# Optimization experiments

Measured on AMD Instinct MI355X. Metric: run time of the kernel, lower is better.

Reference implementation:

```python
import jax, jax.numpy as jnp
import numpy as np
from jax import lax

BN_EPS = 1e-5


def setup_inputs() -> dict:
    key = jax.random.key(0)
    k1, k2 = jax.random.split(key)
    B, C, H, Wd = 32, 256, 56, 56
    x = jax.random.normal(k1, (B, C, H, Wd), dtype=jnp.float32)
    W = jax.random.normal(k2, (C, C, 3, 3), dtype=jnp.float32) * 0.05  # conv weight OIHW
    gamma = jnp.ones((C,), dtype=jnp.float32)
    beta = jnp.zeros((C,), dtype=jnp.float32)
    return {"x": x, "W": W, "gamma": gamma, "beta": beta}


def reference(x, W, gamma, beta):
    # sign activation on input, sign-binarized weights
    s = jnp.sign(x)
    bw = jnp.sign(W)
    # 3x3 conv, stride 1, padding 1 (same spatial size)
    y = lax.conv_general_dilated(
        s, bw,
        window_strides=(1, 1),
        padding=((1, 1), (1, 1)),
        dimension_numbers=("NCHW", "OIHW", "NCHW"),
    )
    # BatchNorm2d in training mode: batch statistics over (N, H, W), biased variance
    mean = jnp.mean(y, axis=(0, 2, 3))
    var = jnp.var(y, axis=(0, 2, 3))
    inv = gamma / jnp.sqrt(var + BN_EPS)
    yn = (y - mean[None, :, None, None]) * inv[None, :, None, None] + beta[None, :, None, None]
    return yn + x
```

## Files before the change

kernel.cpp:

```cpp
#include <hip/hip_runtime.h>
#include <stdint.h>

#define CH 256
#define HWD 56
#define POS 3136
#define BATCH 32
#define PP 3364
#define BN 128
#define NCH 26

typedef unsigned long long u64;
typedef __attribute__((ext_vector_type(4))) int  i32x4;
typedef __attribute__((ext_vector_type(16))) int i32x16;
typedef __attribute__((ext_vector_type(8))) short short8;

#define GLL16(gsrc, ldst) \
    __builtin_amdgcn_global_load_lds((const __attribute__((address_space(1))) void*)(gsrc), \
                                     (__attribute__((address_space(3))) void*)(ldst), 16, 0, 0)

__global__ __launch_bounds__(256) void pack_kernel(
        const float* __restrict__ x, const float* __restrict__ W,
        char* __restrict__ Xp, char* __restrict__ Wb2){
    int blk = blockIdx.x, t = threadIdx.x;
    if (blk < 144){
        int idx = blk*256 + t;
        int cc = idx & 15;
        int ot = idx >> 4;
        int o = ot / 9, tap = ot % 9;
        char v16[16];
        #pragma unroll
        for (int j=0;j<16;j++){
            float v = W[(size_t)(o*CH + cc*16 + j)*9 + tap];
            v16[j] = (v >= 0.f) ? 1 : -1;
        }
        *(int4*)(Wb2 + ((size_t)(tap*16 + cc)*256 + o)*16) = *(int4*)v16;
        return;
    }
    int xb = blk - 144;
    int h = xb % 56, b = xb / 56;
    __shared__ char lds[56][256];
    #pragma unroll
    for (int i = 0; i < 14; ++i){
        int idx = i*256 + t;
        int c = idx / 14, wq = idx - c*14;
        float4 v = *(const float4*)(x + ((size_t)(b*CH + c))*POS + h*HWD + wq*4);
        int w0 = wq*4;
        lds[w0+0][c ^ (((w0+0) & 31) << 2)] = (v.x >= 0.f) ? (char)1 : (char)-1;
        lds[w0+1][c ^ (((w0+1) & 31) << 2)] = (v.y >= 0.f) ? (char)1 : (char)-1;
        lds[w0+2][c ^ (((w0+2) & 31) << 2)] = (v.z >= 0.f) ? (char)1 : (char)-1;
        lds[w0+3][c ^ (((w0+3) & 31) << 2)] = (v.w >= 0.f) ? (char)1 : (char)-1;
    }
    __syncthreads();
    #pragma unroll
    for (int i = 0; i < 4; ++i){
        int idx = t + 256*i;
        if (idx < 896){
            int cc = idx & 15, w = idx >> 4;
            int swz = (w & 31) << 2;
            int4 val;
            val.x = *(const int*)&lds[w][(cc*16 + 0) ^ swz];
            val.y = *(const int*)&lds[w][(cc*16 + 4) ^ swz];
            val.z = *(const int*)&lds[w][(cc*16 + 8) ^ swz];
            val.w = *(const int*)&lds[w][(cc*16 +12) ^ swz];
            int n = b*PP + (h+1)*58 + (w+1);
            *(int4*)(Xp + (size_t)n*256 + ((cc ^ (n & 15)) << 4)) = val;
        }
    }
}

__global__ __launch_bounds__(512) void conv_kernel(
        const char* __restrict__ Xp, const char* __restrict__ Wb2,
        short* __restrict__ y16){
    __shared__ char BL[256*256];
    int blk = blockIdx.x;
    int b = blk / NCH, chunk = blk - b*NCH;
    int n0 = b*PP + 58 + chunk*BN;
    int t = threadIdx.x;
    int wave = t >> 6, l = t & 63;
    int gm = wave & 3, gn = wave >> 2;
    int half = l >> 5, l31 = l & 31;

    const char* src = Xp + (size_t)(n0 - 64)*256;
    #pragma unroll
    for (int i=0;i<8;++i){
        int idx = t + 512*i;
        GLL16(src + (size_t)idx*16, BL + idx*16);
    }
    __syncthreads();

    i32x16 acc[2][2];
    #pragma unroll
    for (int m=0;m<2;++m)
        #pragma unroll
        for (int nt=0;nt<2;++nt)
            #pragma unroll
            for (int r=0;r<16;++r) acc[m][nt][r] = 0;

    int c0 = (n0 - 64) & 15;

    #pragma unroll 1
    for (int tap=0; tap<9; ++tap){
        int off = (tap/3 - 1)*58 + (tap%3 - 1);
        const char* wt = Wb2 + (size_t)tap*65536 + (size_t)half*4096
                             + (size_t)(gm*64 + l31)*16;
        i32x4 afr[2][8];
        #pragma unroll
        for (int m=0;m<2;++m)
            #pragma unroll
            for (int ks=0; ks<8; ++ks)
                afr[m][ks] = *(const i32x4*)(wt + m*512 + ks*8192);
        #pragma unroll
        for (int nt=0; nt<2; ++nt){
            int s = 64 + gn*64 + nt*32 + l31 + off;
            int key = (s + c0) & 15;
            const char* bb = BL + (s << 8);
            #pragma unroll
            for (int ks=0; ks<8; ++ks){
                i32x4 bfr = *(const i32x4*)(bb + (((2*ks + half) ^ key) << 4));
                acc[0][nt] = __builtin_amdgcn_mfma_i32_32x32x32_i8(afr[0][ks], bfr, acc[0][nt], 0,0,0);
                acc[1][nt] = __builtin_amdgcn_mfma_i32_32x32x32_i8(afr[1][ks], bfr, acc[1][nt], 0,0,0);
            }
        }
    }

    #pragma unroll
    for (int nt=0; nt<2; ++nt){
        unsigned nloc = 58 + chunk*BN + gn*64 + nt*32 + l31;
        unsigned hq = nloc / 58;
        unsigned wq = nloc - hq*58;
        bool vok = (hq <= 56) && (wq >= 1) && (wq <= 56);
        if (!vok) continue;
        size_t pbase = (size_t)(hq-1)*HWD + (wq-1);
        #pragma unroll
        for (int m=0;m<2;++m){
            #pragma unroll
            for (int reg=0; reg<16; ++reg){
                int o = gm*64 + m*32 + (reg&3) + 8*(reg>>2) + 4*half;
                y16[(size_t)(b*CH + o)*POS + pbase] = (short)acc[m][nt][reg];
            }
        }
    }
}

__global__ __launch_bounds__(256) void stats_kernel(const short* __restrict__ y16,
                                                    int* __restrict__ sumI, u64* __restrict__ sumQ){
    int o = blockIdx.x, t = threadIdx.x;
    int s = 0; unsigned q = 0;
    for (int b=0; b<BATCH; ++b){
        const short8* yp = (const short8*)(y16 + ((size_t)(b*CH + o))*POS);
        for (int i=t; i<POS/8; i+=256){
            short8 v = yp[i];
            #pragma unroll
            for (int j=0;j<8;++j){ int vv = v[j]; s += vv; q += (unsigned)(vv*vv); }
        }
    }
    long long ls = s, lq = (long long)q;
    #pragma unroll
    for (int off=32; off; off>>=1){
        ls += __shfl_xor(ls, off);
        lq += __shfl_xor(lq, off);
    }
    __shared__ long long wsum[4], wsq[4];
    int wave = t >> 6, lane = t & 63;
    if (lane == 0){ wsum[wave] = ls; wsq[wave] = lq; }
    __syncthreads();
    if (t == 0){
        sumI[o] = (int)(wsum[0]+wsum[1]+wsum[2]+wsum[3]);
        sumQ[o] = (u64)(wsq[0]+wsq[1]+wsq[2]+wsq[3]);
    }
}

__global__ void apply_kernel(const short* __restrict__ y16, const float* __restrict__ x,
                             const int* __restrict__ sumI, const u64* __restrict__ sumQ,
                             const float* __restrict__ gamma, const float* __restrict__ beta,
                             float* __restrict__ out){
    int t = blockIdx.x*blockDim.x + threadIdx.x;
    const int total8 = BATCH*CH*POS/8;
    if (t >= total8) return;
    size_t i = (size_t)t*8;
    int c = (t / (POS/8)) & 255;

    const double N = (double)(BATCH*POS);
    double mean = (double)sumI[c] / N;
    double msq  = (double)sumQ[c] / N;
    double var  = msq - mean*mean;
    double inv  = (double)gamma[c] / sqrt(var + 1e-5);
    float iv = (float)inv;
    float sh = (float)((double)beta[c] - mean*inv);

    short8 yv = *(const short8*)(y16 + i);
    float4 x0 = *(const float4*)(x + i);
    float4 x1 = *(const float4*)(x + i + 4);
    float4 o0, o1;
    o0.x = fmaf((float)yv[0], iv, sh) + x0.x;
    o0.y = fmaf((float)yv[1], iv, sh) + x0.y;
    o0.z = fmaf((float)yv[2], iv, sh) + x0.z;
    o0.w = fmaf((float)yv[3], iv, sh) + x0.w;
    o1.x = fmaf((float)yv[4], iv, sh) + x1.x;
    o1.y = fmaf((float)yv[5], iv, sh) + x1.y;
    o1.z = fmaf((float)yv[6], iv, sh) + x1.z;
    o1.w = fmaf((float)yv[7], iv, sh) + x1.w;
    *(float4*)(out + i)     = o0;
    *(float4*)(out + i + 4) = o1;
}

extern "C" void kernel_launch(void* const* d_in, const int* in_sizes, int n_in,
                              void* d_out, int out_size, void* d_ws, size_t ws_size,
                              hipStream_t stream) {
    const float* x     = (const float*)d_in[0];
    const float* W     = (const float*)d_in[1];
    const float* gamma = (const float*)d_in[2];
    const float* beta  = (const float*)d_in[3];
    float* out = (float*)d_out;

    char* ws = (char*)d_ws;
    short* y16   = (short*)ws;
    char*  Wb2   = (char*)(ws + 51380224);
    int*   sumI  = (int*)(ws + 51970048);
    u64*   sumQ  = (u64*)(ws + 51971072);

    char* Xp = (char*)d_out + 64*256;

    hipMemsetAsync(d_out, 0, (size_t)(64 + 107648 + 128)*256, stream);

    pack_kernel<<<144 + BATCH*HWD, 256, 0, stream>>>(x, W, Xp, Wb2);
    conv_kernel<<<BATCH*NCH, 512, 0, stream>>>(Xp, Wb2, y16);
    stats_kernel<<<CH, 256, 0, stream>>>(y16, sumI, sumQ);
    apply_kernel<<<(BATCH*CH*POS/8 + 255)/256, 256, 0, stream>>>(y16, x, sumI, sumQ, gamma, beta, out);
}
```

Before: 315.7 us.

## Double-buffer conv weight fragments and zero only padding in pack kernel

The conv main loop now walks 36 sub-steps (tap × k-quarter) and loads the next step's weight fragments while the current step's MFMAs run. This cuts live A-fragment registers from 64 to 32 and adds a launch-bounds occupancy hint. The full-buffer hipMemsetAsync of the padded input is replaced by zeroing only the halo rows and columns inside the pack kernel, which removes a large memset pass. The rows before batch 0 are now left uninitialized, but they only feed discarded border outputs.

```diff
diff --git a/kernel.cpp b/kernel.cpp
--- a/kernel.cpp
+++ b/kernel.cpp
@@ -36,7 +36,14 @@
         *(int4*)(Wb2 + ((size_t)(tap*16 + cc)*256 + o)*16) = *(int4*)v16;
         return;
     }
-    int xb = blk - 144;
+    if (blk < 176){
+        int b = blk - 144;
+        int4* r0 = (int4*)(Xp + (size_t)(b*PP)*256);
+        int4* r1 = (int4*)(Xp + (size_t)(b*PP + 57*58)*256);
+        for (int j = t; j < 928; j += 256){ r0[j] = make_int4(0,0,0,0); r1[j] = make_int4(0,0,0,0); }
+        return;
+    }
+    int xb = blk - 176;
     int h = xb % 56, b = xb / 56;
     __shared__ char lds[56][256];
     #pragma unroll
@@ -51,6 +58,10 @@
         lds[w0+3][c ^ (((w0+3) & 31) << 2)] = (v.w >= 0.f) ? (char)1 : (char)-1;
     }
     __syncthreads();
+    if (t < 32){
+        int s = (h+1)*58 + ((t & 1) ? 57 : 0);
+        ((int4*)(Xp + ((size_t)(b*PP + s))*256))[t >> 1] = make_int4(0,0,0,0);
+    }
     #pragma unroll
     for (int i = 0; i < 4; ++i){
         int idx = t + 256*i;
@@ -68,7 +79,30 @@
     }
 }
 
-__global__ __launch_bounds__(512) void conv_kernel(
+#define LOADA(s, r0, r1, r2, r3) { \
+    const char* wp_ = Wb2 + (size_t)((((s)>>2)*16 + ((s)&3)*4 + half)*4096) + abase; \
+    r0 = *(const i32x4*)(wp_);                 \
+    r1 = *(const i32x4*)(wp_ + 512);           \
+    r2 = *(const i32x4*)(wp_ + 8192);          \
+    r3 = *(const i32x4*)(wp_ + 8192 + 512); }
+
+#define COMP(s, r0, r1, r2, r3) { \
+    int tap_ = (s) >> 2, kh_ = (s) & 3; \
+    int off_ = (tap_/3 - 1)*58 + (tap_%3 - 1); \
+    _Pragma("unroll") \
+    for (int nt=0; nt<2; ++nt){ \
+        int sl_ = 64 + gn*64 + nt*32 + l31 + off_; \
+        int key_ = (sl_ + c0) & 15; \
+        const char* bb_ = BL + (sl_ << 8); \
+        i32x4 bf0_ = *(const i32x4*)(bb_ + (((kh_*4 + half) ^ key_) << 4)); \
+        i32x4 bf1_ = *(const i32x4*)(bb_ + (((kh_*4 + 2 + half) ^ key_) << 4)); \
+        acc[0][nt] = __builtin_amdgcn_mfma_i32_32x32x32_i8(r0, bf0_, acc[0][nt], 0,0,0); \
+        acc[1][nt] = __builtin_amdgcn_mfma_i32_32x32x32_i8(r1, bf0_, acc[1][nt], 0,0,0); \
+        acc[0][nt] = __builtin_amdgcn_mfma_i32_32x32x32_i8(r2, bf1_, acc[0][nt], 0,0,0); \
+        acc[1][nt] = __builtin_amdgcn_mfma_i32_32x32x32_i8(r3, bf1_, acc[1][nt], 0,0,0); \
+    } }
+
+__global__ __launch_bounds__(512, 4) void conv_kernel(
         const char* __restrict__ Xp, const char* __restrict__ Wb2,
         short* __restrict__ y16){
     __shared__ char BL[256*256];
@@ -97,30 +131,16 @@
             for (int r=0;r<16;++r) acc[m][nt][r] = 0;
 
     int c0 = (n0 - 64) & 15;
-
+    size_t abase = (size_t)(gm*64 + l31)*16;
+
+    i32x4 p0,p1,p2,p3, q0,q1,q2,q3;
+    LOADA(0, p0,p1,p2,p3);
     #pragma unroll 1
-    for (int tap=0; tap<9; ++tap){
-        int off = (tap/3 - 1)*58 + (tap%3 - 1);
-        const char* wt = Wb2 + (size_t)tap*65536 + (size_t)half*4096
-                             + (size_t)(gm*64 + l31)*16;
-        i32x4 afr[2][8];
-        #pragma unroll
-        for (int m=0;m<2;++m)
-            #pragma unroll
-            for (int ks=0; ks<8; ++ks)
-                afr[m][ks] = *(const i32x4*)(wt + m*512 + ks*8192);
-        #pragma unroll
-        for (int nt=0; nt<2; ++nt){
-            int s = 64 + gn*64 + nt*32 + l31 + off;
-            int key = (s + c0) & 15;
-            const char* bb = BL + (s << 8);
-            #pragma unroll
-            for (int ks=0; ks<8; ++ks){
-                i32x4 bfr = *(const i32x4*)(bb + (((2*ks + half) ^ key) << 4));
-                acc[0][nt] = __builtin_amdgcn_mfma_i32_32x32x32_i8(afr[0][ks], bfr, acc[0][nt], 0,0,0);
-                acc[1][nt] = __builtin_amdgcn_mfma_i32_32x32x32_i8(afr[1][ks], bfr, acc[1][nt], 0,0,0);
-            }
-        }
+    for (int s = 0; s < 36; s += 2){
+        LOADA(s+1, q0,q1,q2,q3);
+        COMP(s, p0,p1,p2,p3);
+        if (s < 34) LOADA(s+2, p0,p1,p2,p3);
+        COMP(s+1, q0,q1,q2,q3);
     }
 
     #pragma unroll
@@ -221,9 +241,7 @@
 
     char* Xp = (char*)d_out + 64*256;
 
-    hipMemsetAsync(d_out, 0, (size_t)(64 + 107648 + 128)*256, stream);
-
-    pack_kernel<<<144 + BATCH*HWD, 256, 0, stream>>>(x, W, Xp, Wb2);
+    pack_kernel<<<144 + 32 + BATCH*HWD, 256, 0, stream>>>(x, W, Xp, Wb2);
     conv_kernel<<<BATCH*NCH, 512, 0, stream>>>(Xp, Wb2, y16);
     stats_kernel<<<CH, 256, 0, stream>>>(y16, sumI, sumQ);
     apply_kernel<<<(BATCH*CH*POS/8 + 255)/256, 256, 0, stream>>>(y16, x, sumI, sumQ, gamma, beta, out);
```

After: 315.3 us. About the same (-0.1%).
